# Performance work log

Hardware: AMD Instinct MI355X
Metric: run time of the kernel (lower is better)

## Reference

```python
import jax, jax.numpy as jnp
import numpy as np

B, N, C, H = 4, 4096, 1024, 16
D = C // H


def setup_inputs() -> dict:
    key = jax.random.key(0)
    ks = jax.random.split(key, 15)
    s = 0.02
    f = lambda k, shp: jax.random.normal(k, shp, dtype=jnp.float32) * s
    return {
        "x": f(ks[0], (B, N, C)),
        "qkv_w": f(ks[1], (C, 3 * C)),
        "qkv_b": f(ks[2], (3 * C,)),
        "out_w": f(ks[3], (C, C)),
        "out_b": f(ks[4], (C,)),
        # NB: original code dynamically re-creates position_bias as (1, N, H, H)
        # because q/k/v are never transposed to (B,H,N,D); attention runs over heads.
        "pos_bias": f(ks[5], (1, N, H, H)),
        "conv_w": f(ks[6], (C, C)),
        "conv_b": f(ks[7], (C,)),
        "pw_w": f(ks[8], (C, C, 1)),   # Conv1d kernel_size=1: (out, in, k)
        "pw_b": f(ks[9], (C,)),
        "dw_w": f(ks[10], (C, 1, 3)),  # depthwise Conv1d groups=C: (out, in/groups=1, k)
        "dw_b": f(ks[11], (C,)),
        "tok_w": f(ks[12], (C, C)),
        "tok_b": f(ks[13], (C,)),
    }


def reference(x, qkv_w, qkv_b, out_w, out_b, pos_bias,
              conv_w, conv_b, pw_w, pw_b, dw_w, dw_b, tok_w, tok_b):
    b, n, c = x.shape
    h = pos_bias.shape[2]
    d = c // h
    scale = d ** (-0.5)

    # ---- attention branch (faithful to source: heads axis is attended over) ----
    qkv = (x @ qkv_w + qkv_b).reshape(b, n, h, 3 * d)
    q, k, v = jnp.split(qkv, 3, axis=-1)  # each (B, N, H, D)
    scores = jnp.einsum("bnhd,bngd->bnhg", q, k) * scale + pos_bias  # (B, N, H, H)
    attn_w = jax.nn.softmax(scores, axis=-1)
    attn = jnp.einsum("bnhg,bngd->bnhd", attn_w, v).reshape(b, n, c)
    attn = attn @ out_w + out_b

    # ---- convolutional branch ----
    xc = x @ conv_w + conv_b            # (B, N, C)
    xc = xc.transpose(0, 2, 1)          # (B, C, N)
    dn = ("NCH", "OIH", "NCH")
    xc = jax.lax.conv_general_dilated(xc, pw_w, (1,), [(0, 0)],
                                      dimension_numbers=dn) + pw_b[None, :, None]
    xc = jax.lax.conv_general_dilated(xc, dw_w, (1,), [(1, 1)],
                                      dimension_numbers=dn,
                                      feature_group_count=c) + dw_b[None, :, None]
    xc = xc.transpose(0, 2, 1) @ tok_w + tok_b  # (B, N, C)

    return attn + xc
```

## Files before the change

kernel.cpp:

```cpp
#include <hip/hip_runtime.h>
#include <hip/hip_bf16.h>


typedef __attribute__((ext_vector_type(8))) short sh8;
typedef __attribute__((ext_vector_type(4))) float f4;

__device__ __forceinline__ float bf2f(short s) {
  unsigned u = ((unsigned)(unsigned short)s) << 16;
  return __builtin_bit_cast(float, u);
}
__device__ __forceinline__ short f2bf(float f) {
  return __builtin_bit_cast(short, __float2bfloat16(f));
}
__device__ __forceinline__ void g2l16(const void* g, void* l) {
  __builtin_amdgcn_global_load_lds(
      (const __attribute__((address_space(1))) unsigned int*)g,
      (__attribute__((address_space(3))) unsigned int*)l, 16, 0, 0);
}

__global__ __launch_bounds__(256) void cvt_f32_bf16(
    const float* __restrict__ src, short* __restrict__ dst, int n8) {
  int i = blockIdx.x * 256 + threadIdx.x;
  if (i >= n8) return;
  float4 a = ((const float4*)src)[i * 2];
  float4 b = ((const float4*)src)[i * 2 + 1];
  sh8 o;
  o[0] = f2bf(a.x); o[1] = f2bf(a.y); o[2] = f2bf(a.z); o[3] = f2bf(a.w);
  o[4] = f2bf(b.x); o[5] = f2bf(b.y); o[6] = f2bf(b.z); o[7] = f2bf(b.w);
  ((sh8*)dst)[i] = o;
}

__global__ __launch_bounds__(256) void transpose_f32_bf16(
    const float* __restrict__ src, short* __restrict__ dst,
    int N, int ldd, int coff) {
  __shared__ float tile[32][33];
  int kb = blockIdx.y * 32, nb = blockIdx.x * 32;
  int tx = threadIdx.x, ty = threadIdx.y;
#pragma unroll
  for (int j = 0; j < 32; j += 8)
    tile[ty + j][tx] = src[(size_t)(kb + ty + j) * N + nb + tx];
  __syncthreads();
#pragma unroll
  for (int j = 0; j < 32; j += 8)
    dst[(size_t)(nb + ty + j) * ldd + coff + kb + tx] = f2bf(tile[tx][ty + j]);
}

__global__ __launch_bounds__(256) void prep_misc(
    const float* __restrict__ pw_w, const float* __restrict__ conv_b,
    const float* __restrict__ pw_b, const float* __restrict__ qkv_b,
    const float* __restrict__ out_b, const float* __restrict__ tok_b,
    const float* __restrict__ dw_w, const float* __restrict__ dw_b,
    float* __restrict__ bias4, float* __restrict__ bcat,
    float* __restrict__ dw0, float* __restrict__ dw1,
    float* __restrict__ dw2, float* __restrict__ dwb) {
  int o = blockIdx.x;
  if (o < 1024) {
    float part = 0.f;
    for (int i = threadIdx.x; i < 1024; i += 256)
      part += pw_w[(size_t)o * 1024 + i] * conv_b[i];
#pragma unroll
    for (int off = 32; off >= 1; off >>= 1) part += __shfl_down(part, off);
    __shared__ float red[4];
    int wid = threadIdx.x >> 6, lane = threadIdx.x & 63;
    if (lane == 0) red[wid] = part;
    __syncthreads();
    if (threadIdx.x == 0) {
      float s = red[0] + red[1] + red[2] + red[3];
      bias4[3072 + o] = s + pw_b[o];
      bcat[o] = out_b[o] + tok_b[o];
      dw0[o] = dw_w[o * 3 + 0];
      dw1[o] = dw_w[o * 3 + 1];
      dw2[o] = dw_w[o * 3 + 2];
      dwb[o] = dw_b[o];
    }
  }
  if (threadIdx.x == 0) bias4[o] = qkv_b[o];
}

template <int OUT_BF16>
__global__ __launch_bounds__(256, 2) void gemm128(
    const short* __restrict__ A, const short* __restrict__ Bt,
    void* __restrict__ Cp, const float* __restrict__ bias, int K, int ldc) {
  __shared__ short As[128 * 32];
  __shared__ short Bs[128 * 32];
  const int wid = threadIdx.x >> 6, lane = threadIdx.x & 63;
  const int bm = blockIdx.y, bn = blockIdx.x;
  const int wr = wid >> 1, wc = wid & 1;
  const size_t abase = (size_t)bm * 128 * K;
  const size_t bbase = (size_t)bn * 128 * K;
  const int r16 = lane & 15, ko = (lane >> 4) * 8;

  f4 acc[4][4] = {};

  for (int k0 = 0; k0 < K; k0 += 32) {
    __syncthreads();
#pragma unroll
    for (int c = 0; c < 2; ++c) {
      int ch = c * 256 + wid * 64 + lane;
      int row = ch >> 2, kc = (ch & 3) * 8;
      g2l16(A + abase + (size_t)row * K + k0 + kc, &As[ch * 8]);
      g2l16(Bt + bbase + (size_t)row * K + k0 + kc, &Bs[ch * 8]);
    }
    __syncthreads();
    sh8 af[4], bf[4];
#pragma unroll
    for (int i = 0; i < 4; ++i)
      af[i] = *(const sh8*)&As[(wr * 64 + i * 16 + r16) * 32 + ko];
#pragma unroll
    for (int j = 0; j < 4; ++j)
      bf[j] = *(const sh8*)&Bs[(wc * 64 + j * 16 + r16) * 32 + ko];
#pragma unroll
    for (int i = 0; i < 4; ++i)
#pragma unroll
      for (int j = 0; j < 4; ++j)
        acc[i][j] = __builtin_amdgcn_mfma_f32_16x16x32_bf16(af[i], bf[j],
                                                            acc[i][j], 0, 0, 0);
  }

  const int crow = wr * 64 + (lane >> 4) * 4;
  const int ccol = wc * 64 + r16;
#pragma unroll
  for (int i = 0; i < 4; ++i) {
#pragma unroll
    for (int j = 0; j < 4; ++j) {
      int col = bn * 128 + ccol + j * 16;
      float bv = bias ? bias[col] : 0.f;
#pragma unroll
      for (int r = 0; r < 4; ++r) {
        int row = bm * 128 + crow + i * 16 + r;
        float v = acc[i][j][r] + bv;
        if (OUT_BF16)
          ((short*)Cp)[(size_t)row * ldc + col] = f2bf(v);
        else
          ((float*)Cp)[(size_t)row * ldc + col] = v;
      }
    }
  }
}

template <int OUT_BF16>
__global__ __launch_bounds__(512, 4) void gemmMain(
    const short* __restrict__ A, const short* __restrict__ Bt,
    void* __restrict__ Cp, const float* __restrict__ bias,
    int K, int ldc, int nbn) {
  __shared__ short lds[36864];
  const int tid = threadIdx.x;
  const int lane = tid & 63, wid = tid >> 6;
  const int wr = wid >> 2, wc = wid & 3;
  const int r16 = lane & 15;
  const int kidx = ((lane >> 4) ^ ((r16 >> 1) & 3)) << 3;

  const int cpx = gridDim.x >> 3;
  const int swz = (blockIdx.x & 7) * cpx + (blockIdx.x >> 3);
  const int bm = swz / nbn, bn = swz % nbn;

  const short* Ag = A + (size_t)bm * 128 * K;
  const short* Bg = Bt + (size_t)bn * 256 * K;

  int gA, lA, gB0, lB0, gB1, lB1;
  {
    int ch = tid, row = ch >> 2;
    int kc = (ch & 3) ^ ((row >> 1) & 3);
    gA = row * K + kc * 8;
    lA = ch * 8;
    int c0 = tid, r0 = c0 >> 2;
    int k0 = (c0 & 3) ^ ((r0 >> 1) & 3);
    gB0 = r0 * K + k0 * 8;
    lB0 = 4096 + c0 * 8;
    int c1 = 512 + tid, r1 = c1 >> 2;
    int k1 = (c1 & 3) ^ ((r1 >> 1) & 3);
    gB1 = r1 * K + k1 * 8;
    lB1 = 4096 + c1 * 8;
  }

  f4 acc[4][4] = {};
  const int NT = K >> 5;

#define STAGE3(KT, BUF)                                     \
  do {                                                      \
    short* lb = &lds[(BUF) * 12288];                        \
    const short* ga = Ag + (KT) * 32;                       \
    const short* gb = Bg + (KT) * 32;                       \
    g2l16(ga + gA, lb + lA);                                \
    g2l16(gb + gB0, lb + lB0);                              \
    g2l16(gb + gB1, lb + lB1);                              \
  } while (0)

  STAGE3(0, 0);
  STAGE3(1, 1);
  asm volatile("s_waitcnt vmcnt(3)" ::: "memory");
  __builtin_amdgcn_sched_barrier(0);
  __builtin_amdgcn_s_barrier();
  __builtin_amdgcn_sched_barrier(0);

  int cb = 0;
  for (int t = 0; t < NT; ++t) {
    int sb = cb + 2; if (sb >= 3) sb -= 3;
    const int kt = (t + 2 < NT) ? t + 2 : 0;
    STAGE3(kt, sb);

    const short* base = &lds[cb * 12288];
    sh8 af[4], bfr[4];
#pragma unroll
    for (int i = 0; i < 4; ++i)
      af[i] = *(const sh8*)&base[(wr * 64 + i * 16 + r16) * 32 + kidx];
#pragma unroll
    for (int j = 0; j < 4; ++j)
      bfr[j] = *(const sh8*)&base[4096 + (wc * 64 + j * 16 + r16) * 32 + kidx];

    __builtin_amdgcn_s_setprio(1);
#pragma unroll
    for (int i = 0; i < 4; ++i)
#pragma unroll
      for (int j = 0; j < 4; ++j)
        acc[i][j] = __builtin_amdgcn_mfma_f32_16x16x32_bf16(af[i], bfr[j],
                                                            acc[i][j], 0, 0, 0);
    __builtin_amdgcn_s_setprio(0);
    __builtin_amdgcn_sched_barrier(0);
    asm volatile("s_waitcnt vmcnt(3)" ::: "memory");
    __builtin_amdgcn_sched_barrier(0);
    __builtin_amdgcn_s_barrier();
    __builtin_amdgcn_sched_barrier(0);
    cb = cb + 1; if (cb >= 3) cb -= 3;
  }
#undef STAGE3

  const int crow0 = bm * 128 + wr * 64 + (lane >> 4) * 4;
  const int ccol0 = bn * 256 + wc * 64 + r16;
  float bv[4];
#pragma unroll
  for (int j = 0; j < 4; ++j) bv[j] = bias ? bias[ccol0 + j * 16] : 0.f;
#pragma unroll
  for (int i = 0; i < 4; ++i) {
#pragma unroll
    for (int r = 0; r < 4; ++r) {
      size_t rowoff = (size_t)(crow0 + i * 16 + r) * ldc + ccol0;
#pragma unroll
      for (int j = 0; j < 4; ++j) {
        float v = acc[i][j][r] + bv[j];
        if (OUT_BF16)
          ((short*)Cp)[rowoff + j * 16] = f2bf(v);
        else
          ((float*)Cp)[rowoff + j * 16] = v;
      }
    }
  }
}

__global__ __launch_bounds__(256) void epilogue(
    const short* __restrict__ qkvx, const float* __restrict__ pos_bias,
    const float* __restrict__ dw0, const float* __restrict__ dw1,
    const float* __restrict__ dw2, const float* __restrict__ dwb,
    short* __restrict__ xcat) {
  __shared__ short sq[4 * 3072];
  __shared__ short slice[6 * 1024];
  int t0 = blockIdx.x * 4;
#pragma unroll
  for (int c = 0; c < 6; ++c) {
    int g = c * 256 + threadIdx.x;
    int tok = (g * 683) >> 18;
    int off = g - tok * 384;
    ((sh8*)sq)[tok * 384 + off] =
        *(const sh8*)(qkvx + (size_t)(t0 + tok) * 4096 + off * 8);
  }
#pragma unroll
  for (int s = 0; s < 3; ++s) {
    int g = s * 256 + threadIdx.x;
    int r = g >> 7, off = g & 127;
    int gr = t0 - 1 + r;
    sh8 v = {};
    if (gr >= 0 && gr < 16384)
      v = *(const sh8*)(qkvx + (size_t)gr * 4096 + 3072 + off * 8);
    ((sh8*)slice)[g] = v;
  }
  __syncthreads();

  int wid = threadIdx.x >> 6, lane = threadIdx.x & 63;
  int t = t0 + wid, n = t & 4095;
  int h = lane >> 2, sub = lane & 3;
  const short* base = sq + wid * 3072 + h * 192;

  float qf[64];
#pragma unroll
  for (int c = 0; c < 8; ++c) {
    sh8 v8 = *(const sh8*)(base + c * 8);
#pragma unroll
    for (int j = 0; j < 8; ++j) qf[c * 8 + j] = bf2f(v8[j]);
  }

  const float* pb = pos_bias + (size_t)n * 256 + h * 16 + sub * 4;
  float p[4];
  float m = -1e30f;
#pragma unroll
  for (int g4 = 0; g4 < 4; ++g4) {
    int g = sub * 4 + g4;
    const short* kk = sq + wid * 3072 + g * 192 + 64;
    float acc = 0.f;
#pragma unroll
    for (int c = 0; c < 8; ++c) {
      sh8 k8 = *(const sh8*)(kk + c * 8);
#pragma unroll
      for (int j = 0; j < 8; ++j) acc += qf[c * 8 + j] * bf2f(k8[j]);
    }
    p[g4] = acc * 0.125f + pb[g4];
    m = fmaxf(m, p[g4]);
  }
  m = fmaxf(m, __shfl_xor(m, 1));
  m = fmaxf(m, __shfl_xor(m, 2));
  float sum = 0.f;
#pragma unroll
  for (int g4 = 0; g4 < 4; ++g4) {
    p[g4] = __expf(p[g4] - m);
    sum += p[g4];
  }
  sum += __shfl_xor(sum, 1);
  sum += __shfl_xor(sum, 2);
  float inv = 1.0f / sum;
#pragma unroll
  for (int g4 = 0; g4 < 4; ++g4) p[g4] *= inv;

  float pall[16];
#pragma unroll
  for (int g = 0; g < 16; ++g)
    pall[g] = __shfl(p[g & 3], (lane & 60) | (g >> 2));

  float o[16] = {};
#pragma unroll
  for (int g = 0; g < 16; ++g) {
    const short* vv = sq + wid * 3072 + g * 192 + 128 + sub * 16;
    sh8 va = *(const sh8*)vv;
    sh8 vb = *(const sh8*)(vv + 8);
#pragma unroll
    for (int j = 0; j < 8; ++j) {
      o[j] += pall[g] * bf2f(va[j]);
      o[8 + j] += pall[g] * bf2f(vb[j]);
    }
  }
  sh8 oa, ob;
#pragma unroll
  for (int j = 0; j < 8; ++j) {
    oa[j] = f2bf(o[j]);
    ob[j] = f2bf(o[8 + j]);
  }
  short* dst = xcat + (size_t)t * 2048 + h * 64 + sub * 16;
  *(sh8*)dst = oa;
  *(sh8*)(dst + 8) = ob;

#pragma unroll
  for (int it = 0; it < 2; ++it) {
    int w = it * 256 + threadIdx.x;
    int tok = w >> 7, co = (w & 127) * 8;
    int tt = t0 + tok, nn = tt & 4095;
    const short* lo8 = slice + tok * 1024 + co;
    const short* mi8 = lo8 + 1024;
    const short* hi8 = lo8 + 2048;
    sh8 lo = (nn > 0) ? *(const sh8*)lo8 : sh8{};
    sh8 mi = *(const sh8*)mi8;
    sh8 hi = (nn < 4095) ? *(const sh8*)hi8 : sh8{};
    sh8 out;
#pragma unroll
    for (int j = 0; j < 8; ++j) {
      float v = dw0[co + j] * bf2f(lo[j]) + dw1[co + j] * bf2f(mi[j]) +
                dw2[co + j] * bf2f(hi[j]) + dwb[co + j];
      out[j] = f2bf(v);
    }
    *(sh8*)(xcat + (size_t)tt * 2048 + 1024 + co) = out;
  }
}

extern "C" void kernel_launch(void* const* d_in, const int* in_sizes, int n_in,
                              void* d_out, int out_size, void* d_ws,
                              size_t ws_size, hipStream_t stream) {
  const float* x      = (const float*)d_in[0];
  const float* qkv_w  = (const float*)d_in[1];
  const float* qkv_b  = (const float*)d_in[2];
  const float* out_w  = (const float*)d_in[3];
  const float* out_b  = (const float*)d_in[4];
  const float* pos_b  = (const float*)d_in[5];
  const float* conv_w = (const float*)d_in[6];
  const float* conv_b = (const float*)d_in[7];
  const float* pw_w   = (const float*)d_in[8];
  const float* pw_b   = (const float*)d_in[9];
  const float* dw_w   = (const float*)d_in[10];
  const float* dw_b   = (const float*)d_in[11];
  const float* tok_w  = (const float*)d_in[12];
  const float* tok_b  = (const float*)d_in[13];

  const int M = 16384;
  char* ws = (char*)d_ws;
  size_t off = 0;
  auto alloc = [&](size_t bytes) -> void* {
    void* p = ws + off;
    off += (bytes + 255) & ~(size_t)255;
    return p;
  };
  short* xb    = (short*)alloc((size_t)M * 1024 * 2);
  short* wbig  = (short*)alloc((size_t)4096 * 1024 * 2);
  short* wcatT = (short*)alloc((size_t)1024 * 2048 * 2);
  short* convb = (short*)alloc((size_t)1024 * 1024 * 2);
  short* pwb   = (short*)alloc((size_t)1024 * 1024 * 2);
  short* qkvx  = (short*)alloc((size_t)M * 4096 * 2);
  short* xcat  = (short*)alloc((size_t)M * 2048 * 2);
  float* bias4 = (float*)alloc(4096 * 4);
  float* bcat  = (float*)alloc(1024 * 4);
  float* dw0   = (float*)alloc(1024 * 4);
  float* dw1   = (float*)alloc(1024 * 4);
  float* dw2   = (float*)alloc(1024 * 4);
  float* dwb   = (float*)alloc(1024 * 4);
  (void)ws_size; (void)in_sizes; (void)n_in; (void)out_size;

  cvt_f32_bf16<<<8192, 256, 0, stream>>>(x, xb, M * 1024 / 8);
  cvt_f32_bf16<<<512, 256, 0, stream>>>(conv_w, convb, 1024 * 1024 / 8);
  cvt_f32_bf16<<<512, 256, 0, stream>>>(pw_w, pwb, 1024 * 1024 / 8);
  transpose_f32_bf16<<<dim3(96, 32), dim3(32, 8), 0, stream>>>(qkv_w, wbig, 3072, 1024, 0);
  transpose_f32_bf16<<<dim3(32, 32), dim3(32, 8), 0, stream>>>(out_w, wcatT, 1024, 2048, 0);
  transpose_f32_bf16<<<dim3(32, 32), dim3(32, 8), 0, stream>>>(tok_w, wcatT, 1024, 2048, 1024);
  prep_misc<<<3072, 256, 0, stream>>>(pw_w, conv_b, pw_b, qkv_b, out_b, tok_b,
                                      dw_w, dw_b, bias4, bcat, dw0, dw1, dw2, dwb);
  gemm128<1><<<dim3(8, 8), 256, 0, stream>>>(pwb, convb, wbig + (size_t)3072 * 1024,
                                             nullptr, 1024, 1024);

  gemmMain<1><<<2048, 512, 0, stream>>>(xb, wbig, qkvx, bias4, 1024, 4096, 16);

  epilogue<<<4096, 256, 0, stream>>>(qkvx, pos_b, dw0, dw1, dw2, dwb, xcat);

  gemmMain<0><<<512, 512, 0, stream>>>(xcat, wcatT, d_out, bcat, 2048, 1024, 4);
}
```

Baseline: 347.3 us.

## Enlarge GEMM tile to 256x256 with 8-phase double-buffered K=64 pipeline

Replaces the 128x256 triple-buffered GEMM with a 256x256 tile kernel that processes K in 64-wide steps, split into four 32-K half-tile phases with interleaved async global-to-LDS loads and barriers. Each wave now holds 8x4 accumulators, which raises arithmetic intensity per LDS and global byte and halves the grid size for both main GEMMs. In exchange it uses 128KB of LDS and more registers, so occupancy drops to 2 blocks per CU. With fewer blocks there is also a risk of tail imbalance, especially on the 256-block output GEMM.

```diff
diff --git a/kernel.cpp b/kernel.cpp
--- a/kernel.cpp
+++ b/kernel.cpp
@@ -139,11 +139,11 @@
 }
 
 template <int OUT_BF16>
-__global__ __launch_bounds__(512, 4) void gemmMain(
+__global__ __launch_bounds__(512, 2) void gemm8p(
     const short* __restrict__ A, const short* __restrict__ Bt,
     void* __restrict__ Cp, const float* __restrict__ bias,
     int K, int ldc, int nbn) {
-  __shared__ short lds[36864];
+  __shared__ short lds[65536];
   const int tid = threadIdx.x;
   const int lane = tid & 63, wid = tid >> 6;
   const int wr = wid >> 2, wc = wid & 3;
@@ -154,60 +154,62 @@
   const int swz = (blockIdx.x & 7) * cpx + (blockIdx.x >> 3);
   const int bm = swz / nbn, bn = swz % nbn;
 
-  const short* Ag = A + (size_t)bm * 128 * K;
+  const short* Ag = A + (size_t)bm * 256 * K;
   const short* Bg = Bt + (size_t)bn * 256 * K;
 
-  int gA, lA, gB0, lB0, gB1, lB1;
+  int goff0, goff1, loff0, loff1;
   {
-    int ch = tid, row = ch >> 2;
-    int kc = (ch & 3) ^ ((row >> 1) & 3);
-    gA = row * K + kc * 8;
-    lA = ch * 8;
-    int c0 = tid, r0 = c0 >> 2;
-    int k0 = (c0 & 3) ^ ((r0 >> 1) & 3);
-    gB0 = r0 * K + k0 * 8;
-    lB0 = 4096 + c0 * 8;
-    int c1 = 512 + tid, r1 = c1 >> 2;
-    int k1 = (c1 & 3) ^ ((r1 >> 1) & 3);
-    gB1 = r1 * K + k1 * 8;
-    lB1 = 4096 + c1 * 8;
-  }
-
-  f4 acc[4][4] = {};
-  const int NT = K >> 5;
-
-#define STAGE3(KT, BUF)                                     \
+    int s0 = tid, row0 = s0 >> 2;
+    int kc0 = (s0 & 3) ^ ((row0 >> 1) & 3);
+    goff0 = row0 * K + kc0 * 8;
+    loff0 = s0 * 8;
+    int s1 = 512 + tid, row1 = s1 >> 2;
+    int kc1 = (s1 & 3) ^ ((row1 >> 1) & 3);
+    goff1 = row1 * K + kc1 * 8;
+    loff1 = s1 * 8;
+  }
+
+  f4 acc[8][4] = {};
+  const int NT = K >> 6;
+
+#define SOP(GB, DS)                                         \
   do {                                                      \
-    short* lb = &lds[(BUF) * 12288];                        \
-    const short* ga = Ag + (KT) * 32;                       \
-    const short* gb = Bg + (KT) * 32;                       \
-    g2l16(ga + gA, lb + lA);                                \
-    g2l16(gb + gB0, lb + lB0);                              \
-    g2l16(gb + gB1, lb + lB1);                              \
+    g2l16((GB) + goff0, (DS) + loff0);                      \
+    g2l16((GB) + goff1, (DS) + loff1);                      \
   } while (0)
 
-  STAGE3(0, 0);
-  STAGE3(1, 1);
-  asm volatile("s_waitcnt vmcnt(3)" ::: "memory");
+  SOP(Ag, &lds[0]);
+  SOP(Bg, &lds[16384]);
+  SOP(Ag + 32, &lds[8192]);
+  SOP(Bg + 32, &lds[24576]);
+  SOP(Ag + 64, &lds[32768]);
+  SOP(Bg + 64, &lds[32768 + 16384]);
+  asm volatile("s_waitcnt vmcnt(6)" ::: "memory");
   __builtin_amdgcn_sched_barrier(0);
   __builtin_amdgcn_s_barrier();
   __builtin_amdgcn_sched_barrier(0);
 
-  int cb = 0;
   for (int t = 0; t < NT; ++t) {
-    int sb = cb + 2; if (sb >= 3) sb -= 3;
-    const int kt = (t + 2 < NT) ? t + 2 : 0;
-    STAGE3(kt, sb);
-
-    const short* base = &lds[cb * 12288];
-    sh8 af[4], bfr[4];
-#pragma unroll
-    for (int i = 0; i < 4; ++i)
-      af[i] = *(const sh8*)&base[(wr * 64 + i * 16 + r16) * 32 + kidx];
+    const int b = t & 1;
+    const short* buf = &lds[b * 32768];
+    short* bufN = &lds[(b ^ 1) * 32768];
+    short* bufC = &lds[b * 32768];
+    const int t1 = (t + 1 < NT) ? t + 1 : 0;
+    const int t2 = (t + 2 < NT) ? t + 2 : 0;
+
+    sh8 af[8], bfr[4];
+
+#pragma unroll
+    for (int i = 0; i < 4; ++i)
+      af[i] = *(const sh8*)&buf[(wr * 128 + i * 16 + r16) * 32 + kidx];
 #pragma unroll
     for (int j = 0; j < 4; ++j)
-      bfr[j] = *(const sh8*)&base[4096 + (wc * 64 + j * 16 + r16) * 32 + kidx];
-
+      bfr[j] = *(const sh8*)&buf[16384 + (wc * 64 + j * 16 + r16) * 32 + kidx];
+    SOP(Ag + t1 * 64 + 32, bufN + 8192);
+    asm volatile("s_waitcnt vmcnt(6)" ::: "memory");
+    __builtin_amdgcn_sched_barrier(0);
+    __builtin_amdgcn_s_barrier();
+    __builtin_amdgcn_sched_barrier(0);
     __builtin_amdgcn_s_setprio(1);
 #pragma unroll
     for (int i = 0; i < 4; ++i)
@@ -217,21 +219,81 @@
                                                             acc[i][j], 0, 0, 0);
     __builtin_amdgcn_s_setprio(0);
     __builtin_amdgcn_sched_barrier(0);
-    asm volatile("s_waitcnt vmcnt(3)" ::: "memory");
-    __builtin_amdgcn_sched_barrier(0);
-    __builtin_amdgcn_s_barrier();
-    __builtin_amdgcn_sched_barrier(0);
-    cb = cb + 1; if (cb >= 3) cb -= 3;
-  }
-#undef STAGE3
-
-  const int crow0 = bm * 128 + wr * 64 + (lane >> 4) * 4;
+    __builtin_amdgcn_s_barrier();
+    __builtin_amdgcn_sched_barrier(0);
+
+#pragma unroll
+    for (int i = 4; i < 8; ++i)
+      af[i] = *(const sh8*)&buf[(wr * 128 + i * 16 + r16) * 32 + kidx];
+    SOP(Bg + t1 * 64 + 32, bufN + 24576);
+    asm volatile("s_waitcnt vmcnt(6)" ::: "memory");
+    __builtin_amdgcn_sched_barrier(0);
+    __builtin_amdgcn_s_barrier();
+    __builtin_amdgcn_sched_barrier(0);
+    __builtin_amdgcn_s_setprio(1);
+#pragma unroll
+    for (int i = 4; i < 8; ++i)
+#pragma unroll
+      for (int j = 0; j < 4; ++j)
+        acc[i][j] = __builtin_amdgcn_mfma_f32_16x16x32_bf16(af[i], bfr[j],
+                                                            acc[i][j], 0, 0, 0);
+    __builtin_amdgcn_s_setprio(0);
+    __builtin_amdgcn_sched_barrier(0);
+    __builtin_amdgcn_s_barrier();
+    __builtin_amdgcn_sched_barrier(0);
+
+#pragma unroll
+    for (int i = 0; i < 4; ++i)
+      af[i] = *(const sh8*)&buf[8192 + (wr * 128 + i * 16 + r16) * 32 + kidx];
+#pragma unroll
+    for (int j = 0; j < 4; ++j)
+      bfr[j] = *(const sh8*)&buf[24576 + (wc * 64 + j * 16 + r16) * 32 + kidx];
+    SOP(Ag + t2 * 64, bufC);
+    asm volatile("s_waitcnt vmcnt(6)" ::: "memory");
+    __builtin_amdgcn_sched_barrier(0);
+    __builtin_amdgcn_s_barrier();
+    __builtin_amdgcn_sched_barrier(0);
+    __builtin_amdgcn_s_setprio(1);
+#pragma unroll
+    for (int i = 0; i < 4; ++i)
+#pragma unroll
+      for (int j = 0; j < 4; ++j)
+        acc[i][j] = __builtin_amdgcn_mfma_f32_16x16x32_bf16(af[i], bfr[j],
+                                                            acc[i][j], 0, 0, 0);
+    __builtin_amdgcn_s_setprio(0);
+    __builtin_amdgcn_sched_barrier(0);
+    __builtin_amdgcn_s_barrier();
+    __builtin_amdgcn_sched_barrier(0);
+
+#pragma unroll
+    for (int i = 4; i < 8; ++i)
+      af[i] = *(const sh8*)&buf[8192 + (wr * 128 + i * 16 + r16) * 32 + kidx];
+    SOP(Bg + t2 * 64, bufC + 16384);
+    asm volatile("s_waitcnt vmcnt(6)" ::: "memory");
+    __builtin_amdgcn_sched_barrier(0);
+    __builtin_amdgcn_s_barrier();
+    __builtin_amdgcn_sched_barrier(0);
+    __builtin_amdgcn_s_setprio(1);
+#pragma unroll
+    for (int i = 4; i < 8; ++i)
+#pragma unroll
+      for (int j = 0; j < 4; ++j)
+        acc[i][j] = __builtin_amdgcn_mfma_f32_16x16x32_bf16(af[i], bfr[j],
+                                                            acc[i][j], 0, 0, 0);
+    __builtin_amdgcn_s_setprio(0);
+    __builtin_amdgcn_sched_barrier(0);
+    __builtin_amdgcn_s_barrier();
+    __builtin_amdgcn_sched_barrier(0);
+  }
+#undef SOP
+
+  const int crow0 = bm * 256 + wr * 128 + (lane >> 4) * 4;
   const int ccol0 = bn * 256 + wc * 64 + r16;
   float bv[4];
 #pragma unroll
   for (int j = 0; j < 4; ++j) bv[j] = bias ? bias[ccol0 + j * 16] : 0.f;
 #pragma unroll
-  for (int i = 0; i < 4; ++i) {
+  for (int i = 0; i < 8; ++i) {
 #pragma unroll
     for (int r = 0; r < 4; ++r) {
       size_t rowoff = (size_t)(crow0 + i * 16 + r) * ldc + ccol0;
@@ -420,9 +482,9 @@
   gemm128<1><<<dim3(8, 8), 256, 0, stream>>>(pwb, convb, wbig + (size_t)3072 * 1024,
                                              nullptr, 1024, 1024);
 
-  gemmMain<1><<<2048, 512, 0, stream>>>(xb, wbig, qkvx, bias4, 1024, 4096, 16);
+  gemm8p<1><<<1024, 512, 0, stream>>>(xb, wbig, qkvx, bias4, 1024, 4096, 16);
 
   epilogue<<<4096, 256, 0, stream>>>(qkvx, pos_b, dw0, dw1, dw2, dwb, xcat);
 
-  gemmMain<0><<<512, 512, 0, stream>>>(xcat, wcatT, d_out, bcat, 2048, 1024, 4);
-}
+  gemm8p<0><<<256, 512, 0, stream>>>(xcat, wcatT, d_out, bcat, 2048, 1024, 4);
+}
```

Result: faster. 331.0 us (-4.7%).
